# Kernel optimization log

Hardware: AMD Instinct MI355X
Metric: run time of the kernel (lower is better)

## Reference

```python
import jax, jax.numpy as jnp
import numpy as np

HORIZONTAL = 4
VERTICAL = 4


def _laplacian3(x):
    """kornia.filters.laplacian(x, kernel_size=3): 3x3 all-ones kernel with
    center -8, normalized by sum(|k|)=16, reflect padding, depthwise conv.
    x: [B, C, H, W] -> [B, C, H, W]."""
    C = x.shape[1]
    k = np.ones((3, 3), dtype=np.float32)
    k[1, 1] = -8.0
    k /= 16.0  # kornia normalized=True
    kern = jnp.asarray(k, dtype=x.dtype)[None, None].repeat(C, axis=0)  # [C,1,3,3]
    xp = jnp.pad(x, ((0, 0), (0, 0), (1, 1), (1, 1)), mode="reflect")
    return jax.lax.conv_general_dilated(
        xp, kern, window_strides=(1, 1), padding="VALID",
        dimension_numbers=("NCHW", "OIHW", "NCHW"), feature_group_count=C)


def setup_inputs() -> dict:
    key = jax.random.key(0)
    k1, k2 = jax.random.split(key)
    shape = (32, 3, 512, 512)
    return {
        "ground_truth_batch": jax.random.normal(k1, shape, dtype=jnp.float32),
        "segmented_print_batch": jax.random.normal(k2, shape, dtype=jnp.float32),
    }


def reference(ground_truth_batch, segmented_print_batch):
    gt_grad = _laplacian3(ground_truth_batch)
    sp_grad = _laplacian3(segmented_print_batch)
    diff = jnp.abs(gt_grad - sp_grad)  # L1, reduction='sum' per block
    B, C, H, W = diff.shape
    vb, hb = H // VERTICAL, W // HORIZONTAL
    # Original code does image.reshape([H, W, C]) (flat reinterpret), then
    # sums |diff| over [vb, hb, C] blocks of that view. Reproduce exactly:
    d = diff.reshape(B, H, W, C)
    blocks = d.reshape(B, VERTICAL, vb, HORIZONTAL, hb, C).sum(axis=(2, 4, 5))  # [B, V, Hz]
    # Per image, keep the max-loss block; total loss = sum over batch.
    return jnp.max(blocks, axis=(1, 2)).sum()
```

## Files before the change

### kernel.cpp

```cpp
#include <hip/hip_runtime.h>

#define HH 512
#define WW 512
#define CC 3
#define BANDS 32
#define BAND_ROWS 16
#define RPW 4
#define NWG (BANDS * CC * 32)
#define NXCD 8


__global__ __launch_bounds__(256, 4) void lap_block_sum_kernel(
    const float* __restrict__ gt, const float* __restrict__ sp,
    float* __restrict__ partial)
{
    __shared__ float ldsr[8][WW];
    __shared__ float red[4][4];

    const int orig = blockIdx.x;
    const int lin  = (orig & (NXCD - 1)) * (NWG / NXCD) + (orig >> 3);
    const int band = lin & (BANDS - 1);
    const int plane = lin >> 5;
    const int c = plane % CC;
    const int b = plane / CC;

    const int t = threadIdx.x;
    const int wv = t >> 6, lane = t & 63;

    const size_t poff = (size_t)plane * (size_t)(HH * WW);
    const float* __restrict__ gtp = gt + poff;
    const float* __restrict__ spp = sp + poff;

    const int h0   = band * BAND_ROWS + wv * RPW;
    const int colA = 4 * lane;
    const int colB = 256 + 4 * lane;

    float hA[4], hB[4];
    {
        int hs = (wv == 0) ? h0 - 1 : h0 + RPW;
        hs = hs < 0 ? 1 : (hs > HH - 1 ? HH - 2 : hs);
        if (wv == 0 || wv == 3) {
            const float* gr = gtp + (size_t)hs * WW;
            const float* sr = spp + (size_t)hs * WW;
            float4 ga = *(const float4*)(gr + colA);
            float4 gb = *(const float4*)(gr + colB);
            float4 sa = *(const float4*)(sr + colA);
            float4 sb = *(const float4*)(sr + colB);
            hA[0]=ga.x-sa.x; hA[1]=ga.y-sa.y; hA[2]=ga.z-sa.z; hA[3]=ga.w-sa.w;
            hB[0]=gb.x-sb.x; hB[1]=gb.y-sb.y; hB[2]=gb.z-sb.z; hB[3]=gb.w-sb.w;
        }
    }

    float dA[RPW][4], dB[RPW][4];
    #pragma unroll
    for (int r = 0; r < RPW; ++r) {
        const float* gr = gtp + (size_t)(h0 + r) * WW;
        const float* sr = spp + (size_t)(h0 + r) * WW;
        float4 ga = *(const float4*)(gr + colA);
        float4 gb = *(const float4*)(gr + colB);
        float4 sa = *(const float4*)(sr + colA);
        float4 sb = *(const float4*)(sr + colB);
        dA[r][0]=ga.x-sa.x; dA[r][1]=ga.y-sa.y; dA[r][2]=ga.z-sa.z; dA[r][3]=ga.w-sa.w;
        dB[r][0]=gb.x-sb.x; dB[r][1]=gb.y-sb.y; dB[r][2]=gb.z-sb.z; dB[r][3]=gb.w-sb.w;
    }

    *(float4*)&ldsr[2*wv  ][colA] = make_float4(dA[0][0],dA[0][1],dA[0][2],dA[0][3]);
    *(float4*)&ldsr[2*wv  ][colB] = make_float4(dB[0][0],dB[0][1],dB[0][2],dB[0][3]);
    *(float4*)&ldsr[2*wv+1][colA] = make_float4(dA[RPW-1][0],dA[RPW-1][1],dA[RPW-1][2],dA[RPW-1][3]);
    *(float4*)&ldsr[2*wv+1][colB] = make_float4(dB[RPW-1][0],dB[RPW-1][1],dB[RPW-1][2],dB[RPW-1][3]);
    __syncthreads();

    float pA[4], pB[4], nA[4], nB[4];
    if (wv == 0) {
        pA[0]=hA[0]; pA[1]=hA[1]; pA[2]=hA[2]; pA[3]=hA[3];
        pB[0]=hB[0]; pB[1]=hB[1]; pB[2]=hB[2]; pB[3]=hB[3];
    } else {
        float4 a = *(const float4*)&ldsr[2*wv-1][colA];
        float4 q = *(const float4*)&ldsr[2*wv-1][colB];
        pA[0]=a.x; pA[1]=a.y; pA[2]=a.z; pA[3]=a.w;
        pB[0]=q.x; pB[1]=q.y; pB[2]=q.z; pB[3]=q.w;
    }
    if (wv == 3) {
        nA[0]=hA[0]; nA[1]=hA[1]; nA[2]=hA[2]; nA[3]=hA[3];
        nB[0]=hB[0]; nB[1]=hB[1]; nB[2]=hB[2]; nB[3]=hB[3];
    } else {
        float4 a = *(const float4*)&ldsr[2*wv+2][colA];
        float4 q = *(const float4*)&ldsr[2*wv+2][colB];
        nA[0]=a.x; nA[1]=a.y; nA[2]=a.z; nA[3]=a.w;
        nB[0]=q.x; nB[1]=q.y; nB[2]=q.z; nB[3]=q.w;
    }

    const int hzA0 = colA/384, hzA1 = (512+colA)/384, hzA2 = (1024+colA)/384;
    const int hzB0 = colB/384, hzB1 = (512+colB)/384, hzB2 = (1024+colB)/384;
    const int lm1 = (lane + 63) & 63, lp1 = (lane + 1) & 63;

    float acc0=0.f, acc1=0.f, acc2=0.f, acc3=0.f;
    int m = (c * HH + h0) % 3;

#define ROWSTEP(TA,TB,RM,BA,BB) do {                                    \
    float csA0 = TA[0]+dA[RM][0]+BA[0];                                 \
    float csA1 = TA[1]+dA[RM][1]+BA[1];                                 \
    float csA2 = TA[2]+dA[RM][2]+BA[2];                                 \
    float csA3 = TA[3]+dA[RM][3]+BA[3];                                 \
    float csB0 = TB[0]+dB[RM][0]+BB[0];                                 \
    float csB1 = TB[1]+dB[RM][1]+BB[1];                                 \
    float csB2 = TB[2]+dB[RM][2]+BB[2];                                 \
    float csB3 = TB[3]+dB[RM][3]+BB[3];                                 \
    float sA3m = __shfl(csA3, lm1), sA0p = __shfl(csA0, lp1);           \
    float sB3m = __shfl(csB3, lm1), sB0p = __shfl(csB0, lp1);           \
    float xR = __shfl(csB0, 0),     xL = __shfl(csA3, 63);              \
    float lA = (lane==0)  ? csA1 : sA3m;   \
    float rA = (lane==63) ? xR   : sA0p;                   \
    float lB = (lane==0)  ? xL   : sB3m;                   \
    float rB = (lane==63) ? csB2 : sB0p;    \
    float sA = fabsf(lA  +csA0+csA1 - 9.f*dA[RM][0])                    \
             + fabsf(csA0+csA1+csA2 - 9.f*dA[RM][1])                    \
             + fabsf(csA1+csA2+csA3 - 9.f*dA[RM][2])                    \
             + fabsf(csA2+csA3+rA   - 9.f*dA[RM][3]);                   \
    float sB = fabsf(lB  +csB0+csB1 - 9.f*dB[RM][0])                    \
             + fabsf(csB0+csB1+csB2 - 9.f*dB[RM][1])                    \
             + fabsf(csB1+csB2+csB3 - 9.f*dB[RM][2])                    \
             + fabsf(csB2+csB3+rB   - 9.f*dB[RM][3]);                   \
    int hzA = (m==0)?hzA0:((m==1)?hzA1:hzA2);                           \
    int hzB = (m==0)?hzB0:((m==1)?hzB1:hzB2);                           \
    acc0 += ((hzA==0)?sA:0.f) + ((hzB==0)?sB:0.f);                      \
    acc1 += ((hzA==1)?sA:0.f) + ((hzB==1)?sB:0.f);                      \
    acc2 += ((hzA==2)?sA:0.f) + ((hzB==2)?sB:0.f);                      \
    acc3 += ((hzA==3)?sA:0.f) + ((hzB==3)?sB:0.f);                      \
    m = (m==2)?0:(m+1);                                                 \
} while(0)

    ROWSTEP(pA,    pB,    0, dA[1], dB[1]);
    ROWSTEP(dA[0], dB[0], 1, dA[2], dB[2]);
    ROWSTEP(dA[1], dB[1], 2, dA[3], dB[3]);
    ROWSTEP(dA[2], dB[2], 3, nA,    nB);
#undef ROWSTEP

    #pragma unroll
    for (int off = 32; off > 0; off >>= 1) {
        acc0 += __shfl_xor(acc0, off);
        acc1 += __shfl_xor(acc1, off);
        acc2 += __shfl_xor(acc2, off);
        acc3 += __shfl_xor(acc3, off);
    }
    if (lane == 0) {
        red[wv][0] = acc0 * 0.0625f; red[wv][1] = acc1 * 0.0625f;
        red[wv][2] = acc2 * 0.0625f; red[wv][3] = acc3 * 0.0625f;
    }
    __syncthreads();
    if (t < 4) {
        partial[lin * 4 + t] = red[0][t] + red[1][t] + red[2][t] + red[3][t];
    }
}

__global__ void finalize_kernel(const float* __restrict__ partial,
                                float* __restrict__ out, int B)
{
    __shared__ float bmax[32];
    const int t = threadIdx.x;
    const int b = t >> 4, v = (t >> 2) & 3, hz = t & 3;
    float s = 0.f;
    if (b < B) {
        #pragma unroll
        for (int c = 0; c < CC; ++c) {
            #pragma unroll
            for (int band = 0; band < BANDS; ++band) {
                if ((c * HH + band * BAND_ROWS) / 384 == v)
                    s += partial[((b * CC + c) * BANDS + band) * 4 + hz];
            }
        }
    }
    #pragma unroll
    for (int off = 8; off > 0; off >>= 1)
        s = fmaxf(s, __shfl_xor(s, off));
    if ((t & 15) == 0) bmax[b] = (b < B) ? s : 0.f;
    __syncthreads();
    if (t < 64) {
        float x = (t < 32) ? bmax[t] : 0.f;
        #pragma unroll
        for (int off = 16; off > 0; off >>= 1)
            x += __shfl_down(x, off);
        if (t == 0) out[0] = x;
    }
}

extern "C" void kernel_launch(void* const* d_in, const int* in_sizes, int n_in,
                              void* d_out, int out_size, void* d_ws, size_t ws_size,
                              hipStream_t stream) {
    const float* gt = (const float*)d_in[0];
    const float* sp = (const float*)d_in[1];
    float* partial = (float*)d_ws;
    float* out = (float*)d_out;

    const int B = in_sizes[0] / (CC * HH * WW);

    lap_block_sum_kernel<<<NWG, 256, 0, stream>>>(gt, sp, partial);

    finalize_kernel<<<1, 512, 0, stream>>>(partial, out, B);
}
```

Before: 49.07 us.

## Process 64-row bands per workgroup with loads overlapped across halves

Each workgroup now covers 64 rows of a plane instead of 16, split into two 32-row halves. Row loads for the second half are interleaved with the stencil compute of the first half, and the LDS row exchange links the two halves. This cuts redundant halo-row reads and the number of workgroups, and hides some memory latency behind arithmetic. In exchange it raises register pressure, drops the occupancy hint, and leaves only a few workgroups per CU.

```diff
diff --git a/kernel.cpp b/kernel.cpp
--- a/kernel.cpp
+++ b/kernel.cpp
@@ -3,26 +3,23 @@
 #define HH 512
 #define WW 512
 #define CC 3
-#define BANDS 32
-#define BAND_ROWS 16
-#define RPW 4
-#define NWG (BANDS * CC * 32)
+#define WGB 8
+#define NWG (WGB * CC * 32)
 #define NXCD 8
 
 
-__global__ __launch_bounds__(256, 4) void lap_block_sum_kernel(
+__global__ __launch_bounds__(256) void lap_block_sum_kernel(
     const float* __restrict__ gt, const float* __restrict__ sp,
     float* __restrict__ partial)
 {
-    __shared__ float ldsr[8][WW];
+    __shared__ float ldsr[16][WW];
     __shared__ float red[4][4];
 
     const int orig = blockIdx.x;
     const int lin  = (orig & (NXCD - 1)) * (NWG / NXCD) + (orig >> 3);
-    const int band = lin & (BANDS - 1);
-    const int plane = lin >> 5;
+    const int wgband = lin & (WGB - 1);
+    const int plane  = lin >> 3;
     const int c = plane % CC;
-    const int b = plane / CC;
 
     const int t = threadIdx.x;
     const int wv = t >> 6, lane = t & 63;
@@ -31,63 +28,59 @@
     const float* __restrict__ gtp = gt + poff;
     const float* __restrict__ spp = sp + poff;
 
-    const int h0   = band * BAND_ROWS + wv * RPW;
+    const int start = wgband * 64;
+    const int h1 = start + wv * 8;
+    const int h2 = start + 32 + wv * 8;
     const int colA = 4 * lane;
     const int colB = 256 + 4 * lane;
 
+#define LOADDIFF(HS, DA, DB) do {                                   \
+    const float* gr_ = gtp + (size_t)(HS) * WW;                     \
+    const float* sr_ = spp + (size_t)(HS) * WW;                     \
+    float4 ga_ = *(const float4*)(gr_ + colA);                      \
+    float4 gb_ = *(const float4*)(gr_ + colB);                      \
+    float4 sa_ = *(const float4*)(sr_ + colA);                      \
+    float4 sb_ = *(const float4*)(sr_ + colB);                      \
+    DA[0]=ga_.x-sa_.x; DA[1]=ga_.y-sa_.y;                           \
+    DA[2]=ga_.z-sa_.z; DA[3]=ga_.w-sa_.w;                           \
+    DB[0]=gb_.x-sb_.x; DB[1]=gb_.y-sb_.y;                           \
+    DB[2]=gb_.z-sb_.z; DB[3]=gb_.w-sb_.w;                           \
+} while (0)
+
     float hA[4], hB[4];
-    {
-        int hs = (wv == 0) ? h0 - 1 : h0 + RPW;
-        hs = hs < 0 ? 1 : (hs > HH - 1 ? HH - 2 : hs);
-        if (wv == 0 || wv == 3) {
-            const float* gr = gtp + (size_t)hs * WW;
-            const float* sr = spp + (size_t)hs * WW;
-            float4 ga = *(const float4*)(gr + colA);
-            float4 gb = *(const float4*)(gr + colB);
-            float4 sa = *(const float4*)(sr + colA);
-            float4 sb = *(const float4*)(sr + colB);
-            hA[0]=ga.x-sa.x; hA[1]=ga.y-sa.y; hA[2]=ga.z-sa.z; hA[3]=ga.w-sa.w;
-            hB[0]=gb.x-sb.x; hB[1]=gb.y-sb.y; hB[2]=gb.z-sb.z; hB[3]=gb.w-sb.w;
-        }
-    }
-
-    float dA[RPW][4], dB[RPW][4];
+    if (wv == 0 || wv == 3) {
+        int hs = (wv == 0) ? (start == 0 ? 1 : start - 1) : (start + 32);
+        LOADDIFF(hs, hA, hB);
+    }
+
+    float d1A[8][4], d1B[8][4];
     #pragma unroll
-    for (int r = 0; r < RPW; ++r) {
-        const float* gr = gtp + (size_t)(h0 + r) * WW;
-        const float* sr = spp + (size_t)(h0 + r) * WW;
-        float4 ga = *(const float4*)(gr + colA);
-        float4 gb = *(const float4*)(gr + colB);
-        float4 sa = *(const float4*)(sr + colA);
-        float4 sb = *(const float4*)(sr + colB);
-        dA[r][0]=ga.x-sa.x; dA[r][1]=ga.y-sa.y; dA[r][2]=ga.z-sa.z; dA[r][3]=ga.w-sa.w;
-        dB[r][0]=gb.x-sb.x; dB[r][1]=gb.y-sb.y; dB[r][2]=gb.z-sb.z; dB[r][3]=gb.w-sb.w;
-    }
-
-    *(float4*)&ldsr[2*wv  ][colA] = make_float4(dA[0][0],dA[0][1],dA[0][2],dA[0][3]);
-    *(float4*)&ldsr[2*wv  ][colB] = make_float4(dB[0][0],dB[0][1],dB[0][2],dB[0][3]);
-    *(float4*)&ldsr[2*wv+1][colA] = make_float4(dA[RPW-1][0],dA[RPW-1][1],dA[RPW-1][2],dA[RPW-1][3]);
-    *(float4*)&ldsr[2*wv+1][colB] = make_float4(dB[RPW-1][0],dB[RPW-1][1],dB[RPW-1][2],dB[RPW-1][3]);
-    __syncthreads();
-
-    float pA[4], pB[4], nA[4], nB[4];
+    for (int r = 0; r < 8; ++r) LOADDIFF(h1 + r, d1A[r], d1B[r]);
+
+    *(float4*)&ldsr[2*wv  ][colA] = *(const float4*)&d1A[0][0];
+    *(float4*)&ldsr[2*wv  ][colB] = *(const float4*)&d1B[0][0];
+    *(float4*)&ldsr[2*wv+1][colA] = *(const float4*)&d1A[7][0];
+    *(float4*)&ldsr[2*wv+1][colB] = *(const float4*)&d1B[7][0];
+    __syncthreads();
+
+    float p1A[4], p1B[4], n1A[4], n1B[4];
     if (wv == 0) {
-        pA[0]=hA[0]; pA[1]=hA[1]; pA[2]=hA[2]; pA[3]=hA[3];
-        pB[0]=hB[0]; pB[1]=hB[1]; pB[2]=hB[2]; pB[3]=hB[3];
+        #pragma unroll
+        for (int i = 0; i < 4; ++i) { p1A[i]=hA[i]; p1B[i]=hB[i]; }
     } else {
         float4 a = *(const float4*)&ldsr[2*wv-1][colA];
         float4 q = *(const float4*)&ldsr[2*wv-1][colB];
-        pA[0]=a.x; pA[1]=a.y; pA[2]=a.z; pA[3]=a.w;
-        pB[0]=q.x; pB[1]=q.y; pB[2]=q.z; pB[3]=q.w;
+        p1A[0]=a.x;p1A[1]=a.y;p1A[2]=a.z;p1A[3]=a.w;
+        p1B[0]=q.x;p1B[1]=q.y;p1B[2]=q.z;p1B[3]=q.w;
     }
     if (wv == 3) {
-        nA[0]=hA[0]; nA[1]=hA[1]; nA[2]=hA[2]; nA[3]=hA[3];
-        nB[0]=hB[0]; nB[1]=hB[1]; nB[2]=hB[2]; nB[3]=hB[3];
+        #pragma unroll
+        for (int i = 0; i < 4; ++i) { n1A[i]=hA[i]; n1B[i]=hB[i]; }
     } else {
         float4 a = *(const float4*)&ldsr[2*wv+2][colA];
         float4 q = *(const float4*)&ldsr[2*wv+2][colB];
-        nA[0]=a.x; nA[1]=a.y; nA[2]=a.z; nA[3]=a.w;
-        nB[0]=q.x; nB[1]=q.y; nB[2]=q.z; nB[3]=q.w;
+        n1A[0]=a.x;n1A[1]=a.y;n1A[2]=a.z;n1A[3]=a.w;
+        n1B[0]=q.x;n1B[1]=q.y;n1B[2]=q.z;n1B[3]=q.w;
     }
 
     const int hzA0 = colA/384, hzA1 = (512+colA)/384, hzA2 = (1024+colA)/384;
@@ -95,17 +88,16 @@
     const int lm1 = (lane + 63) & 63, lp1 = (lane + 1) & 63;
 
     float acc0=0.f, acc1=0.f, acc2=0.f, acc3=0.f;
-    int m = (c * HH + h0) % 3;
-
-#define ROWSTEP(TA,TB,RM,BA,BB) do {                                    \
-    float csA0 = TA[0]+dA[RM][0]+BA[0];                                 \
-    float csA1 = TA[1]+dA[RM][1]+BA[1];                                 \
-    float csA2 = TA[2]+dA[RM][2]+BA[2];                                 \
-    float csA3 = TA[3]+dA[RM][3]+BA[3];                                 \
-    float csB0 = TB[0]+dB[RM][0]+BB[0];                                 \
-    float csB1 = TB[1]+dB[RM][1]+BB[1];                                 \
-    float csB2 = TB[2]+dB[RM][2]+BB[2];                                 \
-    float csB3 = TB[3]+dB[RM][3]+BB[3];                                 \
+
+#define ROWSTEP(DDA,DDB,TA,TB,RM,BA,BB) do {                            \
+    float csA0 = TA[0]+DDA[RM][0]+BA[0];                                \
+    float csA1 = TA[1]+DDA[RM][1]+BA[1];                                \
+    float csA2 = TA[2]+DDA[RM][2]+BA[2];                                \
+    float csA3 = TA[3]+DDA[RM][3]+BA[3];                                \
+    float csB0 = TB[0]+DDB[RM][0]+BB[0];                                \
+    float csB1 = TB[1]+DDB[RM][1]+BB[1];                                \
+    float csB2 = TB[2]+DDB[RM][2]+BB[2];                                \
+    float csB3 = TB[3]+DDB[RM][3]+BB[3];                                \
     float sA3m = __shfl(csA3, lm1), sA0p = __shfl(csA0, lp1);           \
     float sB3m = __shfl(csB3, lm1), sB0p = __shfl(csB0, lp1);           \
     float xR = __shfl(csB0, 0),     xL = __shfl(csA3, 63);              \
@@ -113,14 +105,14 @@
     float rA = (lane==63) ? xR   : sA0p;                   \
     float lB = (lane==0)  ? xL   : sB3m;                   \
     float rB = (lane==63) ? csB2 : sB0p;    \
-    float sA = fabsf(lA  +csA0+csA1 - 9.f*dA[RM][0])                    \
-             + fabsf(csA0+csA1+csA2 - 9.f*dA[RM][1])                    \
-             + fabsf(csA1+csA2+csA3 - 9.f*dA[RM][2])                    \
-             + fabsf(csA2+csA3+rA   - 9.f*dA[RM][3]);                   \
-    float sB = fabsf(lB  +csB0+csB1 - 9.f*dB[RM][0])                    \
-             + fabsf(csB0+csB1+csB2 - 9.f*dB[RM][1])                    \
-             + fabsf(csB1+csB2+csB3 - 9.f*dB[RM][2])                    \
-             + fabsf(csB2+csB3+rB   - 9.f*dB[RM][3]);                   \
+    float sA = fabsf(lA  +csA0+csA1 - 9.f*DDA[RM][0])                   \
+             + fabsf(csA0+csA1+csA2 - 9.f*DDA[RM][1])                   \
+             + fabsf(csA1+csA2+csA3 - 9.f*DDA[RM][2])                   \
+             + fabsf(csA2+csA3+rA   - 9.f*DDA[RM][3]);                  \
+    float sB = fabsf(lB  +csB0+csB1 - 9.f*DDB[RM][0])                   \
+             + fabsf(csB0+csB1+csB2 - 9.f*DDB[RM][1])                   \
+             + fabsf(csB1+csB2+csB3 - 9.f*DDB[RM][2])                   \
+             + fabsf(csB2+csB3+rB   - 9.f*DDB[RM][3]);                  \
     int hzA = (m==0)?hzA0:((m==1)?hzA1:hzA2);                           \
     int hzB = (m==0)?hzB0:((m==1)?hzB1:hzB2);                           \
     acc0 += ((hzA==0)?sA:0.f) + ((hzB==0)?sB:0.f);                      \
@@ -130,11 +122,67 @@
     m = (m==2)?0:(m+1);                                                 \
 } while(0)
 
-    ROWSTEP(pA,    pB,    0, dA[1], dB[1]);
-    ROWSTEP(dA[0], dB[0], 1, dA[2], dB[2]);
-    ROWSTEP(dA[1], dB[1], 2, dA[3], dB[3]);
-    ROWSTEP(dA[2], dB[2], 3, nA,    nB);
+    float d2A[8][4], d2B[8][4];
+    float h3A[4], h3B[4];
+    if (wv == 3) {
+        int hs = (start + 64 > HH - 1) ? HH - 2 : start + 64;
+        LOADDIFF(hs, h3A, h3B);
+    }
+
+    int m = (c * HH + h1) % 3;
+
+    LOADDIFF(h2 + 0, d2A[0], d2B[0]);
+    ROWSTEP(d1A,d1B, p1A,   p1B,   0, d1A[1], d1B[1]);
+    LOADDIFF(h2 + 1, d2A[1], d2B[1]);
+    ROWSTEP(d1A,d1B, d1A[0],d1B[0], 1, d1A[2], d1B[2]);
+    LOADDIFF(h2 + 2, d2A[2], d2B[2]);
+    ROWSTEP(d1A,d1B, d1A[1],d1B[1], 2, d1A[3], d1B[3]);
+    LOADDIFF(h2 + 3, d2A[3], d2B[3]);
+    ROWSTEP(d1A,d1B, d1A[2],d1B[2], 3, d1A[4], d1B[4]);
+    LOADDIFF(h2 + 4, d2A[4], d2B[4]);
+    ROWSTEP(d1A,d1B, d1A[3],d1B[3], 4, d1A[5], d1B[5]);
+    LOADDIFF(h2 + 5, d2A[5], d2B[5]);
+    ROWSTEP(d1A,d1B, d1A[4],d1B[4], 5, d1A[6], d1B[6]);
+    LOADDIFF(h2 + 6, d2A[6], d2B[6]);
+    ROWSTEP(d1A,d1B, d1A[5],d1B[5], 6, d1A[7], d1B[7]);
+    LOADDIFF(h2 + 7, d2A[7], d2B[7]);
+    ROWSTEP(d1A,d1B, d1A[6],d1B[6], 7, n1A,    n1B);
+
+    *(float4*)&ldsr[8+2*wv  ][colA] = *(const float4*)&d2A[0][0];
+    *(float4*)&ldsr[8+2*wv  ][colB] = *(const float4*)&d2B[0][0];
+    *(float4*)&ldsr[8+2*wv+1][colA] = *(const float4*)&d2A[7][0];
+    *(float4*)&ldsr[8+2*wv+1][colB] = *(const float4*)&d2B[7][0];
+    __syncthreads();
+
+    float p2A[4], p2B[4], n2A[4], n2B[4];
+    {
+        const int ps = (wv == 0) ? 7 : (8 + 2*wv - 1);
+        float4 a = *(const float4*)&ldsr[ps][colA];
+        float4 q = *(const float4*)&ldsr[ps][colB];
+        p2A[0]=a.x;p2A[1]=a.y;p2A[2]=a.z;p2A[3]=a.w;
+        p2B[0]=q.x;p2B[1]=q.y;p2B[2]=q.z;p2B[3]=q.w;
+    }
+    if (wv == 3) {
+        #pragma unroll
+        for (int i = 0; i < 4; ++i) { n2A[i]=h3A[i]; n2B[i]=h3B[i]; }
+    } else {
+        float4 a = *(const float4*)&ldsr[8+2*wv+2][colA];
+        float4 q = *(const float4*)&ldsr[8+2*wv+2][colB];
+        n2A[0]=a.x;n2A[1]=a.y;n2A[2]=a.z;n2A[3]=a.w;
+        n2B[0]=q.x;n2B[1]=q.y;n2B[2]=q.z;n2B[3]=q.w;
+    }
+
+    m = (c * HH + h2) % 3;
+    ROWSTEP(d2A,d2B, p2A,   p2B,   0, d2A[1], d2B[1]);
+    ROWSTEP(d2A,d2B, d2A[0],d2B[0], 1, d2A[2], d2B[2]);
+    ROWSTEP(d2A,d2B, d2A[1],d2B[1], 2, d2A[3], d2B[3]);
+    ROWSTEP(d2A,d2B, d2A[2],d2B[2], 3, d2A[4], d2B[4]);
+    ROWSTEP(d2A,d2B, d2A[3],d2B[3], 4, d2A[5], d2B[5]);
+    ROWSTEP(d2A,d2B, d2A[4],d2B[4], 5, d2A[6], d2B[6]);
+    ROWSTEP(d2A,d2B, d2A[5],d2B[5], 6, d2A[7], d2B[7]);
+    ROWSTEP(d2A,d2B, d2A[6],d2B[6], 7, n2A,    n2B);
 #undef ROWSTEP
+#undef LOADDIFF
 
     #pragma unroll
     for (int off = 32; off > 0; off >>= 1) {
@@ -164,9 +212,9 @@
         #pragma unroll
         for (int c = 0; c < CC; ++c) {
             #pragma unroll
-            for (int band = 0; band < BANDS; ++band) {
-                if ((c * HH + band * BAND_ROWS) / 384 == v)
-                    s += partial[((b * CC + c) * BANDS + band) * 4 + hz];
+            for (int band = 0; band < WGB; ++band) {
+                if ((c * HH + band * 64) / 384 == v)
+                    s += partial[((b * CC + c) * WGB + band) * 4 + hz];
             }
         }
     }
```

After: 40.78 us (median of 2 runs). 16.9% less time.
